# Kernel tuning notes

Hardware: AMD Instinct MI355X
Metric: run time of the kernel (lower is better)

The kernel has to match this reference:

```python
import jax, jax.numpy as jnp
import numpy as np

B, N, D, H, W = 2, 6, 120, 32, 88
C = 128
Z, HO, WO = 1, 128, 128  # bev_feat_shape
N_POINTS = 1_000_000


def setup_inputs() -> dict:
    key = jax.random.key(0)
    k1, k2, k3, k4, k5 = jax.random.split(key, 5)
    depth = jax.random.normal(k1, (B, N, D, H, W), dtype=jnp.float32)
    feat = jax.random.normal(k2, (B, N, C, H, W), dtype=jnp.float32)
    ranks_depth = jax.random.randint(k3, (N_POINTS,), 0, B * N * D * H * W, dtype=jnp.int32)
    ranks_feat = jax.random.randint(k4, (N_POINTS,), 0, B * N * H * W, dtype=jnp.int32)
    ranks_bev = jnp.sort(jax.random.randint(k5, (N_POINTS,), 0, B * Z * HO * WO, dtype=jnp.int32))
    # Derive intervals (consecutive runs of equal ranks_bev), as the CUDA op expects.
    rb = np.asarray(ranks_bev)
    starts = np.concatenate([[0], np.nonzero(np.diff(rb))[0] + 1]).astype(np.int32)
    lengths = np.diff(np.concatenate([starts, [rb.shape[0]]])).astype(np.int32)
    return {
        "depth": depth,
        "feat": feat,
        "ranks_depth": ranks_depth,
        "ranks_feat": ranks_feat,
        "ranks_bev": ranks_bev,
        "interval_starts": jnp.asarray(starts),
        "interval_lengths": jnp.asarray(lengths),
    }


def reference(depth, feat, ranks_depth, ranks_feat, ranks_bev, interval_starts, interval_lengths):
    b, n, c, h, w = feat.shape
    # feat laid out [b,n,c,h,w]; ranks_feat indexes (b,n,h,w) positions -> put c last.
    feat_flat = feat.transpose(0, 1, 3, 4, 2).reshape(-1, c)  # [b*n*h*w, c]
    depth_flat = depth.reshape(-1)                            # [b*n*d*h*w]
    # Gather depth scalar and feature row per point, multiply.
    prod = depth_flat[ranks_depth][:, None] * feat_flat[ranks_feat]  # [n_points, c]
    # Interval-based accumulation == segment-sum over sorted ranks_bev.
    num_cells = b * Z * HO * WO
    out = jax.ops.segment_sum(prod, ranks_bev, num_segments=num_cells)  # [b*z*h*w, c]
    out = out.reshape(b, Z, HO, WO, c).transpose(0, 4, 1, 2, 3)  # [b, c, z, h, w]
    return out
```

## Files before the change

kernel.cpp:

```cpp
#include <hip/hip_runtime.h>
#include <hip/hip_bf16.h>

#define HW_    2816
#define C_     128
#define BN_    12
#define SPAT_  16384
#define CELLS_ 32768

#define TF_BX     88
#define TF_BY     4
#define TF_BLOCKS (TF_BX * TF_BY * BN_)
#define PG_BLOCKS 1024
#define IV_BLOCKS 128
#define ZB_BLOCKS 512

__device__ __forceinline__ unsigned int f2bf_rne(float x) {
    const unsigned int u = __float_as_uint(x);
    return (u + 0x7fffu + ((u >> 16) & 1u)) >> 16;
}

__global__ __launch_bounds__(256) void prep_k(
        const float* __restrict__ feat, __hip_bfloat16* __restrict__ featT,
        const float* __restrict__ depth, const int* __restrict__ rd,
        const int* __restrict__ rf, unsigned int* __restrict__ pair, int n_points,
        const int* __restrict__ istart, const int* __restrict__ ilen,
        const int* __restrict__ rb, int4* __restrict__ iv4, int n_intervals,
        uint4* __restrict__ zbuf, int zb_n16) {
    __shared__ float tile[32][33];
    const int bid = blockIdx.x;
    const int tid = threadIdx.x;

    if (bid < TF_BLOCKS) {
        const int bn  = bid / (TF_BX * TF_BY);
        const int r   = bid - bn * (TF_BX * TF_BY);
        const int c0  = (r / TF_BX) * 32;
        const int hw0 = (r - (r / TF_BX) * TF_BX) * 32;
        const int x = tid & 31, y = tid >> 5;
        const float* src = feat + ((size_t)bn * C_ + c0) * HW_ + hw0;
        #pragma unroll
        for (int yy = y; yy < 32; yy += 8)
            tile[yy][x] = src[(size_t)yy * HW_ + x];
        __syncthreads();
        __hip_bfloat16* dst = featT + ((size_t)bn * HW_ + hw0) * C_ + c0;
        #pragma unroll
        for (int yy = y; yy < 32; yy += 8)
            dst[(size_t)yy * C_ + x] = __float2bfloat16(tile[x][yy]);
    } else if (bid < TF_BLOCKS + PG_BLOCKS) {
        const int t = (bid - TF_BLOCKS) * 256 + tid;
        const int stride = PG_BLOCKS * 256;
        for (int base = t; base < n_points; base += 4 * stride) {
            int ii[4], idx[4], rfv[4];
            float v[4];
            #pragma unroll
            for (int u = 0; u < 4; ++u) {
                ii[u] = base + u * stride;
                const int cl = ii[u] < n_points ? ii[u] : base;
                idx[u] = rd[cl];
                rfv[u] = rf[cl];
            }
            #pragma unroll
            for (int u = 0; u < 4; ++u) v[u] = depth[idx[u]];
            #pragma unroll
            for (int u = 0; u < 4; ++u)
                if (ii[u] < n_points)
                    pair[ii[u]] = (f2bf_rne(v[u]) << 16) | (unsigned)rfv[u];
        }
    } else if (bid < TF_BLOCKS + PG_BLOCKS + IV_BLOCKS) {
        const int ivl = (bid - TF_BLOCKS - PG_BLOCKS) * 256 + tid;
        if (ivl < n_intervals) {
            const int s = istart[ivl];
            iv4[ivl] = make_int4(s, ilen[ivl], rb[s], 0);
        }
    } else {
        int i = (bid - TF_BLOCKS - PG_BLOCKS - IV_BLOCKS) * 256 + tid;
        for (; i < zb_n16; i += ZB_BLOCKS * 256)
            zbuf[i] = make_uint4(0u, 0u, 0u, 0u);
    }
}

__global__ __launch_bounds__(256) void bevpool_half_k(
        const unsigned int* __restrict__ pair,
        const uint4* __restrict__ featT,
        const int4* __restrict__ iv4,
        unsigned short* __restrict__ cellbuf,
        int n_intervals) {
    const int half = blockIdx.x & 1;
    const int widx = threadIdx.x >> 6;
    const int ivl  = (blockIdx.x >> 1) * 4 + widx;
    if (ivl >= n_intervals) return;
    const int lane = threadIdx.x & 63;
    const int grp  = lane >> 3;
    const int sl   = lane & 7;

    const int4 v    = iv4[ivl];
    const int start = v.x;
    const int end   = v.x + v.y;
    const int cell  = v.z;

    float acc[8] = {0.f, 0.f, 0.f, 0.f, 0.f, 0.f, 0.f, 0.f};
    const size_t hoff = (size_t)(half * 8 + sl);

    for (int i = start + grp; i < end; i += 32) {
        int cl_[4];
        unsigned pr_[4];
        float d_[4];
        uint4 f_[4];
        #pragma unroll
        for (int u = 0; u < 4; ++u) {
            const int ii = i + 8 * u;
            cl_[u] = (ii < end) ? ii : i;
        }
        #pragma unroll
        for (int u = 0; u < 4; ++u) pr_[u] = pair[cl_[u]];
        #pragma unroll
        for (int u = 0; u < 4; ++u) d_[u] = __uint_as_float(pr_[u] & 0xffff0000u);
        #pragma unroll
        for (int u = 1; u < 4; ++u) d_[u] = (i + 8 * u < end) ? d_[u] : 0.f;
        #pragma unroll
        for (int u = 0; u < 4; ++u)
            f_[u] = featT[(size_t)(pr_[u] & 0xffffu) * 16 + hoff];
        #pragma unroll
        for (int u = 0; u < 4; ++u) {
            const float d = d_[u];
            acc[0] = fmaf(d, __uint_as_float(f_[u].x << 16),         acc[0]);
            acc[1] = fmaf(d, __uint_as_float(f_[u].x & 0xffff0000u), acc[1]);
            acc[2] = fmaf(d, __uint_as_float(f_[u].y << 16),         acc[2]);
            acc[3] = fmaf(d, __uint_as_float(f_[u].y & 0xffff0000u), acc[3]);
            acc[4] = fmaf(d, __uint_as_float(f_[u].z << 16),         acc[4]);
            acc[5] = fmaf(d, __uint_as_float(f_[u].z & 0xffff0000u), acc[5]);
            acc[6] = fmaf(d, __uint_as_float(f_[u].w << 16),         acc[6]);
            acc[7] = fmaf(d, __uint_as_float(f_[u].w & 0xffff0000u), acc[7]);
        }
    }

    #pragma unroll
    for (int c = 0; c < 8; ++c) {
        acc[c] += __shfl_down(acc[c], 32);
        acc[c] += __shfl_down(acc[c], 16);
        acc[c] += __shfl_down(acc[c], 8);
    }

    if (grp == 0) {
        uint4 p;
        p.x = f2bf_rne(acc[0]) | (f2bf_rne(acc[1]) << 16);
        p.y = f2bf_rne(acc[2]) | (f2bf_rne(acc[3]) << 16);
        p.z = f2bf_rne(acc[4]) | (f2bf_rne(acc[5]) << 16);
        p.w = f2bf_rne(acc[6]) | (f2bf_rne(acc[7]) << 16);
        *(uint4*)(cellbuf + (size_t)cell * C_ + half * 64 + sl * 8) = p;
    }
}

__global__ __launch_bounds__(256) void transpose_out_bf16_k(const unsigned short* __restrict__ cellbuf,
                                                            float* __restrict__ out) {
    __shared__ float tile[32][33];
    const int b   = blockIdx.z;
    const int sp0 = blockIdx.x * 32;
    const int c0  = blockIdx.y * 32;
    const int x = threadIdx.x;
    const int y = threadIdx.y;

    const unsigned short* src = cellbuf + ((size_t)b * SPAT_ + sp0) * C_ + c0;
    #pragma unroll
    for (int yy = y; yy < 32; yy += 8)
        tile[yy][x] = __uint_as_float((unsigned int)src[(size_t)yy * C_ + x] << 16);
    __syncthreads();
    float* dst = out + ((size_t)b * C_ + c0) * SPAT_ + sp0;
    #pragma unroll
    for (int yy = y; yy < 32; yy += 8)
        dst[(size_t)yy * SPAT_ + x] = tile[x][yy];
}

__global__ __launch_bounds__(256) void bevpool_fallback_k(const float* __restrict__ depth,
                                                          const float* __restrict__ feat,
                                                          const int* __restrict__ rd_arr,
                                                          const int* __restrict__ rf_arr,
                                                          const int* __restrict__ rb,
                                                          const int* __restrict__ istart,
                                                          const int* __restrict__ ilen,
                                                          float* __restrict__ out,
                                                          int n_intervals) {
    const int wave = (int)((blockIdx.x * blockDim.x + threadIdx.x) >> 6);
    const int lane = threadIdx.x & 63;
    if (wave >= n_intervals) return;
    const int start = istart[wave];
    const int len   = ilen[wave];
    const int cell  = rb[start];
    float ax = 0.f, ay = 0.f;
    const int end = start + len;
    for (int i = start; i < end; ++i) {
        const int rfi = rf_arr[i];
        const int bn  = rfi / HW_;
        const int hw  = rfi - bn * HW_;
        const float d = depth[rd_arr[i]];
        const float* frow = feat + (size_t)bn * (C_ * HW_) + hw;
        ax = fmaf(d, frow[(size_t)(2 * lane)     * HW_], ax);
        ay = fmaf(d, frow[(size_t)(2 * lane + 1) * HW_], ay);
    }
    const int b  = cell >> 14;
    const int sp = cell & (SPAT_ - 1);
    float* o = out + (size_t)b * ((size_t)C_ * SPAT_) + sp;
    o[(size_t)(2 * lane)     * SPAT_] = ax;
    o[(size_t)(2 * lane + 1) * SPAT_] = ay;
}

extern "C" void kernel_launch(void* const* d_in, const int* in_sizes, int n_in,
                              void* d_out, int out_size, void* d_ws, size_t ws_size,
                              hipStream_t stream) {
    const float* depth  = (const float*)d_in[0];
    const float* feat   = (const float*)d_in[1];
    const int*   rd     = (const int*)d_in[2];
    const int*   rf     = (const int*)d_in[3];
    const int*   rb     = (const int*)d_in[4];
    const int*   istart = (const int*)d_in[5];
    const int*   ilen   = (const int*)d_in[6];
    float*       out    = (float*)d_out;
    const int n_intervals = in_sizes[5];
    const int n_points    = in_sizes[2];

    const size_t cellbuf_bytes = (size_t)CELLS_ * C_ * sizeof(unsigned short);
    const size_t featT_bytes   = (size_t)BN_ * HW_ * C_ * sizeof(__hip_bfloat16);
    const size_t pair_bytes    = ((size_t)n_points * sizeof(unsigned int) + 15) & ~(size_t)15;
    const size_t iv4_bytes     = (size_t)CELLS_ * sizeof(int4);

    if (ws_size >= cellbuf_bytes + featT_bytes + pair_bytes + iv4_bytes &&
        n_intervals <= CELLS_) {
        unsigned short* cellbuf = (unsigned short*)d_ws;
        __hip_bfloat16* featT   = (__hip_bfloat16*)((char*)d_ws + cellbuf_bytes);
        unsigned int*   pair    = (unsigned int*)((char*)d_ws + cellbuf_bytes + featT_bytes);
        int4*           iv4     = (int4*)((char*)d_ws + cellbuf_bytes + featT_bytes + pair_bytes);

        const int prep_blocks = TF_BLOCKS + PG_BLOCKS + IV_BLOCKS + ZB_BLOCKS;
        prep_k<<<prep_blocks, 256, 0, stream>>>(
            feat, featT, depth, rd, rf, pair, n_points,
            istart, ilen, rb, iv4, n_intervals,
            (uint4*)cellbuf, (int)(cellbuf_bytes / 16));

        const int blocks2 = 2 * ((n_intervals + 3) / 4);
        bevpool_half_k<<<blocks2, 256, 0, stream>>>(
            pair, (const uint4*)featT, iv4, cellbuf, n_intervals);

        {
            dim3 g(SPAT_ / 32, C_ / 32, 2);
            dim3 b(32, 8);
            transpose_out_bf16_k<<<g, b, 0, stream>>>(cellbuf, out);
        }
    } else {
        hipMemsetAsync(out, 0, (size_t)out_size * sizeof(float), stream);
        const int blocks = (n_intervals + 3) / 4;
        bevpool_fallback_k<<<blocks, 256, 0, stream>>>(
            depth, feat, rd, rf, rb, istart, ilen, out, n_intervals);
    }
}
```

Before: 63.32 us.

## Fuse segment-sum with output transpose via cell-to-interval map and LDS staging

Builds a cell-to-interval map in the prep kernel so each block can own a contiguous range of 64 BEV cells. That block accumulates its intervals in fp32, stages them in LDS and writes the transposed [b,c,h,w] output directly. This drops the bf16 intermediate cell buffer, its zero-fill and the separate transpose kernel, and removes the bf16 rounding of accumulated results. In exchange each block carries a serial loop over four cells per wave, and the map fill loops over gaps between cells.

```diff
diff --git a/kernel.cpp b/kernel.cpp
--- a/kernel.cpp
+++ b/kernel.cpp
@@ -6,13 +6,13 @@
 #define BN_    12
 #define SPAT_  16384
 #define CELLS_ 32768
+#define CB_    64
 
 #define TF_BX     88
 #define TF_BY     4
 #define TF_BLOCKS (TF_BX * TF_BY * BN_)
 #define PG_BLOCKS 1024
 #define IV_BLOCKS 128
-#define ZB_BLOCKS 512
 
 __device__ __forceinline__ unsigned int f2bf_rne(float x) {
     const unsigned int u = __float_as_uint(x);
@@ -24,8 +24,8 @@
         const float* __restrict__ depth, const int* __restrict__ rd,
         const int* __restrict__ rf, unsigned int* __restrict__ pair, int n_points,
         const int* __restrict__ istart, const int* __restrict__ ilen,
-        const int* __restrict__ rb, int4* __restrict__ iv4, int n_intervals,
-        uint4* __restrict__ zbuf, int zb_n16) {
+        const int* __restrict__ rb, int4* __restrict__ iv4,
+        int* __restrict__ map, int n_intervals) {
     __shared__ float tile[32][33];
     const int bid = blockIdx.x;
     const int tid = threadIdx.x;
@@ -65,109 +65,111 @@
                 if (ii[u] < n_points)
                     pair[ii[u]] = (f2bf_rne(v[u]) << 16) | (unsigned)rfv[u];
         }
-    } else if (bid < TF_BLOCKS + PG_BLOCKS + IV_BLOCKS) {
+    } else {
         const int ivl = (bid - TF_BLOCKS - PG_BLOCKS) * 256 + tid;
         if (ivl < n_intervals) {
             const int s = istart[ivl];
-            iv4[ivl] = make_int4(s, ilen[ivl], rb[s], 0);
-        }
-    } else {
-        int i = (bid - TF_BLOCKS - PG_BLOCKS - IV_BLOCKS) * 256 + tid;
-        for (; i < zb_n16; i += ZB_BLOCKS * 256)
-            zbuf[i] = make_uint4(0u, 0u, 0u, 0u);
-    }
-}
-
-__global__ __launch_bounds__(256) void bevpool_half_k(
+            const int c = rb[s];
+            iv4[ivl] = make_int4(s, ilen[ivl], c, 0);
+            map[c] = ivl;
+            const int cnext = (ivl + 1 < n_intervals) ? rb[istart[ivl + 1]] : CELLS_;
+            for (int cc = c + 1; cc < cnext; ++cc) map[cc] = -1;
+            if (ivl == 0) for (int cc = 0; cc < c; ++cc) map[cc] = -1;
+        }
+    }
+}
+
+__global__ __launch_bounds__(1024, 4) void bevpool_cells_k(
         const unsigned int* __restrict__ pair,
         const uint4* __restrict__ featT,
         const int4* __restrict__ iv4,
-        unsigned short* __restrict__ cellbuf,
-        int n_intervals) {
-    const int half = blockIdx.x & 1;
-    const int widx = threadIdx.x >> 6;
-    const int ivl  = (blockIdx.x >> 1) * 4 + widx;
-    if (ivl >= n_intervals) return;
-    const int lane = threadIdx.x & 63;
+        const int* __restrict__ map,
+        float* __restrict__ out) {
+    __shared__ float lds[CB_][68];
+    const int half  = blockIdx.x & 1;
+    const int cb    = blockIdx.x >> 1;
+    const int cell0 = cb * CB_;
+    const int tid   = threadIdx.x;
+
+    #pragma unroll
+    for (int i = tid; i < CB_ * 68; i += 1024) (&lds[0][0])[i] = 0.f;
+    __syncthreads();
+
+    const int widx = tid >> 6;
+    const int lane = tid & 63;
     const int grp  = lane >> 3;
     const int sl   = lane & 7;
-
-    const int4 v    = iv4[ivl];
-    const int start = v.x;
-    const int end   = v.x + v.y;
-    const int cell  = v.z;
-
-    float acc[8] = {0.f, 0.f, 0.f, 0.f, 0.f, 0.f, 0.f, 0.f};
     const size_t hoff = (size_t)(half * 8 + sl);
-
-    for (int i = start + grp; i < end; i += 32) {
-        int cl_[4];
-        unsigned pr_[4];
-        float d_[4];
-        uint4 f_[4];
+    const int cl0  = widx * 4;
+
+    const int4 m4 = *(const int4*)&map[cell0 + cl0];
+    const int m[4] = {m4.x, m4.y, m4.z, m4.w};
+    int4 vq[4];
+    #pragma unroll
+    for (int q = 0; q < 4; ++q) vq[q] = iv4[m[q] < 0 ? 0 : m[q]];
+
+    #pragma unroll
+    for (int q = 0; q < 4; ++q) {
+        if (m[q] < 0) continue;
+        const int start = vq[q].x;
+        const int end   = vq[q].x + vq[q].y;
+
+        float acc[8] = {0.f, 0.f, 0.f, 0.f, 0.f, 0.f, 0.f, 0.f};
+        for (int i = start + grp; i < end; i += 32) {
+            int cl_[4];
+            unsigned pr_[4];
+            float d_[4];
+            uint4 f_[4];
+            #pragma unroll
+            for (int u = 0; u < 4; ++u) {
+                const int ii = i + 8 * u;
+                cl_[u] = (ii < end) ? ii : i;
+            }
+            #pragma unroll
+            for (int u = 0; u < 4; ++u) pr_[u] = pair[cl_[u]];
+            #pragma unroll
+            for (int u = 0; u < 4; ++u) d_[u] = __uint_as_float(pr_[u] & 0xffff0000u);
+            #pragma unroll
+            for (int u = 1; u < 4; ++u) d_[u] = (i + 8 * u < end) ? d_[u] : 0.f;
+            #pragma unroll
+            for (int u = 0; u < 4; ++u)
+                f_[u] = featT[(size_t)(pr_[u] & 0xffffu) * 16 + hoff];
+            #pragma unroll
+            for (int u = 0; u < 4; ++u) {
+                const float d = d_[u];
+                acc[0] = fmaf(d, __uint_as_float(f_[u].x << 16),         acc[0]);
+                acc[1] = fmaf(d, __uint_as_float(f_[u].x & 0xffff0000u), acc[1]);
+                acc[2] = fmaf(d, __uint_as_float(f_[u].y << 16),         acc[2]);
+                acc[3] = fmaf(d, __uint_as_float(f_[u].y & 0xffff0000u), acc[3]);
+                acc[4] = fmaf(d, __uint_as_float(f_[u].z << 16),         acc[4]);
+                acc[5] = fmaf(d, __uint_as_float(f_[u].z & 0xffff0000u), acc[5]);
+                acc[6] = fmaf(d, __uint_as_float(f_[u].w << 16),         acc[6]);
+                acc[7] = fmaf(d, __uint_as_float(f_[u].w & 0xffff0000u), acc[7]);
+            }
+        }
         #pragma unroll
-        for (int u = 0; u < 4; ++u) {
-            const int ii = i + 8 * u;
-            cl_[u] = (ii < end) ? ii : i;
-        }
-        #pragma unroll
-        for (int u = 0; u < 4; ++u) pr_[u] = pair[cl_[u]];
-        #pragma unroll
-        for (int u = 0; u < 4; ++u) d_[u] = __uint_as_float(pr_[u] & 0xffff0000u);
-        #pragma unroll
-        for (int u = 1; u < 4; ++u) d_[u] = (i + 8 * u < end) ? d_[u] : 0.f;
-        #pragma unroll
-        for (int u = 0; u < 4; ++u)
-            f_[u] = featT[(size_t)(pr_[u] & 0xffffu) * 16 + hoff];
-        #pragma unroll
-        for (int u = 0; u < 4; ++u) {
-            const float d = d_[u];
-            acc[0] = fmaf(d, __uint_as_float(f_[u].x << 16),         acc[0]);
-            acc[1] = fmaf(d, __uint_as_float(f_[u].x & 0xffff0000u), acc[1]);
-            acc[2] = fmaf(d, __uint_as_float(f_[u].y << 16),         acc[2]);
-            acc[3] = fmaf(d, __uint_as_float(f_[u].y & 0xffff0000u), acc[3]);
-            acc[4] = fmaf(d, __uint_as_float(f_[u].z << 16),         acc[4]);
-            acc[5] = fmaf(d, __uint_as_float(f_[u].z & 0xffff0000u), acc[5]);
-            acc[6] = fmaf(d, __uint_as_float(f_[u].w << 16),         acc[6]);
-            acc[7] = fmaf(d, __uint_as_float(f_[u].w & 0xffff0000u), acc[7]);
-        }
-    }
-
-    #pragma unroll
-    for (int c = 0; c < 8; ++c) {
-        acc[c] += __shfl_down(acc[c], 32);
-        acc[c] += __shfl_down(acc[c], 16);
-        acc[c] += __shfl_down(acc[c], 8);
-    }
-
-    if (grp == 0) {
-        uint4 p;
-        p.x = f2bf_rne(acc[0]) | (f2bf_rne(acc[1]) << 16);
-        p.y = f2bf_rne(acc[2]) | (f2bf_rne(acc[3]) << 16);
-        p.z = f2bf_rne(acc[4]) | (f2bf_rne(acc[5]) << 16);
-        p.w = f2bf_rne(acc[6]) | (f2bf_rne(acc[7]) << 16);
-        *(uint4*)(cellbuf + (size_t)cell * C_ + half * 64 + sl * 8) = p;
-    }
-}
-
-__global__ __launch_bounds__(256) void transpose_out_bf16_k(const unsigned short* __restrict__ cellbuf,
-                                                            float* __restrict__ out) {
-    __shared__ float tile[32][33];
-    const int b   = blockIdx.z;
-    const int sp0 = blockIdx.x * 32;
-    const int c0  = blockIdx.y * 32;
-    const int x = threadIdx.x;
-    const int y = threadIdx.y;
-
-    const unsigned short* src = cellbuf + ((size_t)b * SPAT_ + sp0) * C_ + c0;
-    #pragma unroll
-    for (int yy = y; yy < 32; yy += 8)
-        tile[yy][x] = __uint_as_float((unsigned int)src[(size_t)yy * C_ + x] << 16);
+        for (int c = 0; c < 8; ++c) {
+            acc[c] += __shfl_down(acc[c], 32);
+            acc[c] += __shfl_down(acc[c], 16);
+            acc[c] += __shfl_down(acc[c], 8);
+        }
+        if (grp == 0) {
+            #pragma unroll
+            for (int c = 0; c < 8; ++c) lds[cl0 + q][sl * 8 + c] = acc[c];
+        }
+    }
     __syncthreads();
-    float* dst = out + ((size_t)b * C_ + c0) * SPAT_ + sp0;
-    #pragma unroll
-    for (int yy = y; yy < 32; yy += 8)
-        dst[(size_t)yy * SPAT_ + x] = tile[x][yy];
+
+    const int cl  = tid & 63;
+    const int chb = tid >> 6;
+    const int b   = cell0 >> 14;
+    const int sp0 = cell0 & (SPAT_ - 1);
+    float* obase = out + ((size_t)b * C_ + half * 64) * SPAT_ + sp0;
+    #pragma unroll
+    for (int it = 0; it < 4; ++it) {
+        const int ch = chb + 16 * it;
+        obase[(size_t)ch * SPAT_ + cl] = lds[cl][ch];
+    }
 }
 
 __global__ __launch_bounds__(256) void bevpool_fallback_k(const float* __restrict__ depth,
@@ -217,33 +219,25 @@
     const int n_intervals = in_sizes[5];
     const int n_points    = in_sizes[2];
 
-    const size_t cellbuf_bytes = (size_t)CELLS_ * C_ * sizeof(unsigned short);
-    const size_t featT_bytes   = (size_t)BN_ * HW_ * C_ * sizeof(__hip_bfloat16);
-    const size_t pair_bytes    = ((size_t)n_points * sizeof(unsigned int) + 15) & ~(size_t)15;
-    const size_t iv4_bytes     = (size_t)CELLS_ * sizeof(int4);
-
-    if (ws_size >= cellbuf_bytes + featT_bytes + pair_bytes + iv4_bytes &&
+    const size_t featT_bytes = (size_t)BN_ * HW_ * C_ * sizeof(__hip_bfloat16);
+    const size_t pair_bytes  = ((size_t)n_points * sizeof(unsigned int) + 15) & ~(size_t)15;
+    const size_t iv4_bytes   = (size_t)CELLS_ * sizeof(int4);
+    const size_t map_bytes   = (size_t)CELLS_ * sizeof(int);
+
+    if (ws_size >= featT_bytes + pair_bytes + iv4_bytes + map_bytes &&
         n_intervals <= CELLS_) {
-        unsigned short* cellbuf = (unsigned short*)d_ws;
-        __hip_bfloat16* featT   = (__hip_bfloat16*)((char*)d_ws + cellbuf_bytes);
-        unsigned int*   pair    = (unsigned int*)((char*)d_ws + cellbuf_bytes + featT_bytes);
-        int4*           iv4     = (int4*)((char*)d_ws + cellbuf_bytes + featT_bytes + pair_bytes);
-
-        const int prep_blocks = TF_BLOCKS + PG_BLOCKS + IV_BLOCKS + ZB_BLOCKS;
+        __hip_bfloat16* featT = (__hip_bfloat16*)d_ws;
+        unsigned int*   pair  = (unsigned int*)((char*)d_ws + featT_bytes);
+        int4*           iv4   = (int4*)((char*)d_ws + featT_bytes + pair_bytes);
+        int*            map   = (int*)((char*)d_ws + featT_bytes + pair_bytes + iv4_bytes);
+
+        const int prep_blocks = TF_BLOCKS + PG_BLOCKS + IV_BLOCKS;
         prep_k<<<prep_blocks, 256, 0, stream>>>(
             feat, featT, depth, rd, rf, pair, n_points,
-            istart, ilen, rb, iv4, n_intervals,
-            (uint4*)cellbuf, (int)(cellbuf_bytes / 16));
-
-        const int blocks2 = 2 * ((n_intervals + 3) / 4);
-        bevpool_half_k<<<blocks2, 256, 0, stream>>>(
-            pair, (const uint4*)featT, iv4, cellbuf, n_intervals);
-
-        {
-            dim3 g(SPAT_ / 32, C_ / 32, 2);
-            dim3 b(32, 8);
-            transpose_out_bf16_k<<<g, b, 0, stream>>>(cellbuf, out);
-        }
+            istart, ilen, rb, iv4, map, n_intervals);
+
+        bevpool_cells_k<<<(CELLS_ / CB_) * 2, 1024, 0, stream>>>(
+            pair, (const uint4*)featT, iv4, map, out);
     } else {
         hipMemsetAsync(out, 0, (size_t)out_size * sizeof(float), stream);
         const int blocks = (n_intervals + 3) / 4;
```

Result: faster. 59.03 us, median of 2 (-6.8%).
